# Optimization experiments

Measured on AMD Instinct MI355X. Metric: run time of the kernel, lower is better.

Reference implementation:

```python
import jax, jax.numpy as jnp
import numpy as np

VERIFY_OP = 0  # protocol['operations','verify']
YES = 0        # protocol['concepts','yes']
NO = 1         # protocol['concepts','no']
EMBED_DIM = 16


def _act(x):
    # torch.clamp(x, -1, 5) + 0.1 * x
    return jnp.clip(x, -1.0, 5.0) + 0.1 * x


def setup_inputs() -> dict:
    key = jax.random.key(0)
    ks = jax.random.split(key, 6)
    B, O, Fd, C, L, E = 32, 64, 512, 512, 16, EMBED_DIM
    D2 = 2 * E * E  # 512
    scene = jax.random.normal(ks[0], (B, O, Fd), jnp.float32)
    program_ops = jax.random.randint(ks[1], (B, L), 0, 4)
    program_concepts = jax.random.randint(ks[2], (B, L), 0, C)
    concept_table = jax.random.normal(ks[3], (C, D2), jnp.float32) * 0.02
    feat_W = jax.random.normal(ks[4], (D2, Fd), jnp.float32) * 0.02
    feat_b = jax.random.normal(ks[5], (D2,), jnp.float32) * 0.02
    return {"scene": scene, "program_ops": program_ops,
            "program_concepts": program_concepts, "concept_table": concept_table,
            "feat_W": feat_W, "feat_b": feat_b}


def reference(scene, program_ops, program_concepts, concept_table, feat_W, feat_b):
    B, O, Fd = scene.shape
    C, D2 = concept_table.shape
    E = EMBED_DIM
    sq = E * E
    N = C + O  # num_nodes = max_concepts + num_objects

    # feature_linear on all scenes (all scenes full -> embed_init rows overwritten)
    objects = jnp.einsum('bof,df->bod', scene, feat_W) + feat_b  # [B,O,2sq]
    concepts = jnp.broadcast_to(concept_table[None], (B, C, D2))
    all_nodes = jnp.concatenate([concepts, objects], axis=1)  # [B,N,2sq]
    n1 = all_nodes[..., :sq].reshape(B, N, E, E)
    n2 = all_nodes[..., sq:].reshape(B, N, E, E)
    nodes = jnp.einsum('bnij,bnjk->bnik', n1, n2)  # [B,N,E,E]
    exp_nodes = nodes.reshape(B, N, sq)

    args_emb = concept_table[program_concepts]  # [B,L,2sq]
    L = args_emb.shape[1]
    g1 = args_emb[..., :sq].reshape(B, L, E, E).transpose(1, 0, 2, 3)  # [L,B,E,E]
    g2 = args_emb[..., sq:].reshape(B, L, E, E).transpose(1, 0, 2, 3)
    ops = program_ops.T  # [L,B]

    def step(att, xs):
        a1, a2, op = xs
        # matmul(a1^T, nodes, a2) per node
        wm = jnp.einsum('bji,bnjk,bkl->bnil', a1, nodes, a2).reshape(B, N, sq)
        em = wm * att[:, :, None]
        sim = jnp.einsum('bnd,bmd->bnm', em, exp_nodes)  # [B,N,N]
        if_verify = _act(sim[:, :, YES] - sim[:, :, NO])  # [B,N]
        if_transfer = _act(sim.sum(axis=1))               # [B,N]
        is_verify = (op == VERIFY_OP).astype(att.dtype)[:, None]
        new_att = is_verify * if_verify + (1.0 - is_verify) * if_transfer
        return new_att, new_att

    att0 = jnp.ones((B, N), scene.dtype)
    att, history = jax.lax.scan(step, att0, (g1, g2, ops))
    return jax.nn.log_softmax(att, axis=1), history
```

## Files before the change

kernel.cpp:

```cpp
#include <hip/hip_runtime.h>

#define Bb 32
#define Oo 64
#define FD 512
#define Cc 512
#define Ll 16
#define SQ 256
#define D2 512
#define NN 576
#define QQ 6
#define NPB 96
#define NPW 12
#define STAG 17u

typedef __attribute__((ext_vector_type(8))) short short8v;
typedef __attribute__((ext_vector_type(4))) float f32x4;
typedef unsigned long long u64;

__device__ inline unsigned short bf16_rne(float f) {
  unsigned u = __builtin_bit_cast(unsigned, f);
  unsigned r = (u + 0x7fffu + ((u >> 16) & 1u)) >> 16;
  return (unsigned short)r;
}
__device__ inline float bf16_to_f(unsigned short h) {
  unsigned u = ((unsigned)h) << 16;
  return __builtin_bit_cast(float, u);
}
__device__ inline u64 pack_tag(float v, unsigned tag) {
  return ((u64)__float_as_uint(v) << 32) | (u64)tag;
}

__global__ __launch_bounds__(256) void prep(const float* __restrict__ W,
                                            unsigned short* __restrict__ WH,
                                            unsigned short* __restrict__ WL,
                                            u64* __restrict__ slotG,
                                            u64* __restrict__ slotS) {
  const int gid = blockIdx.x * 256 + threadIdx.x;
#pragma unroll
  for (int k = 0; k < 2; ++k) {
    const int i = gid * 2 + k;
    if (i < Bb * QQ * 2 * SQ)
      __hip_atomic_store(&slotG[i], 0ULL, __ATOMIC_RELAXED, __HIP_MEMORY_SCOPE_AGENT);
  }
  if (gid < Bb * QQ * 2)
    __hip_atomic_store(&slotS[gid], 0ULL, __ATOMIC_RELAXED, __HIP_MEMORY_SCOPE_AGENT);
  const float4 v = ((const float4*)W)[gid];
  float vv[4] = {v.x, v.y, v.z, v.w};
  unsigned short hh[4], ll[4];
#pragma unroll
  for (int j = 0; j < 4; ++j) {
    unsigned short hb = bf16_rne(vv[j]);
    float rem = vv[j] - bf16_to_f(hb);
    hh[j] = hb;
    ll[j] = bf16_rne(rem);
  }
  ushort4 h, lo;
  h.x = hh[0]; h.y = hh[1]; h.z = hh[2]; h.w = hh[3];
  lo.x = ll[0]; lo.y = ll[1]; lo.z = ll[2]; lo.w = ll[3];
  ((ushort4*)WH)[gid] = h;
  ((ushort4*)WL)[gid] = lo;
}

__global__ __launch_bounds__(256) void gemm_nodes(const float* __restrict__ scene,
                                                  const unsigned short* __restrict__ WH,
                                                  const unsigned short* __restrict__ WL,
                                                  const float* __restrict__ bias,
                                                  const float* __restrict__ ct,
                                                  float* __restrict__ cn,
                                                  float* __restrict__ on) {
  __shared__ __align__(16) float sbuf[16 * 529 + 512];
  const int bid = blockIdx.x, tid = threadIdx.x;
  if (bid >= 128) {
    float* ls = sbuf;
    const int c0 = (bid - 128) * 8;
    for (int i = tid; i < 1024; i += 256)
      ((float4*)ls)[i] = ((const float4*)(ct + (size_t)c0 * D2))[i];
    __syncthreads();
    const int n = tid >> 5, sub = tid & 31;
    const float* n1 = &ls[n * 512];
    const float* n2 = &ls[n * 512 + 256];
    float* dst = cn + (size_t)(c0 + n) * SQ + sub * 8;
#pragma unroll
    for (int j = 0; j < 8; ++j) {
      const int e = sub * 8 + j, i = e >> 4, k = e & 15;
      float s = 0.f;
#pragma unroll
      for (int t = 0; t < 16; ++t) s += n1[i * 16 + t] * n2[t * 16 + k];
      dst[j] = s;
    }
    return;
  }
  float (*objLds)[529] = (float(*)[529])sbuf;
  float* biasL = sbuf + 16 * 529;
  const int wave = tid >> 6, lane = tid & 63;
  const int rowbase = bid * 16;
  for (int i = tid; i < 512; i += 256) biasL[i] = bias[i];

  const int ar = lane & 15;
  const int koff = (lane >> 4) * 8;
  const float* Arow = scene + (size_t)(rowbase + ar) * FD;
  const int ncol0 = wave * 128;
  f32x4 acc[8];
#pragma unroll
  for (int i = 0; i < 8; ++i) acc[i] = (f32x4){0.f, 0.f, 0.f, 0.f};

  for (int k0 = 0; k0 < FD; k0 += 32) {
    float a[8];
    *(float4*)&a[0] = *(const float4*)&Arow[k0 + koff];
    *(float4*)&a[4] = *(const float4*)&Arow[k0 + koff + 4];
    short8v ah, al;
#pragma unroll
    for (int j = 0; j < 8; ++j) {
      unsigned short hb = bf16_rne(a[j]);
      float rem = a[j] - bf16_to_f(hb);
      ah[j] = (short)hb;
      al[j] = (short)bf16_rne(rem);
    }
#pragma unroll
    for (int ni = 0; ni < 8; ++ni) {
      const int d = ncol0 + ni * 16 + ar;
      const short8v wh = *(const short8v*)&WH[(size_t)d * FD + k0 + koff];
      const short8v wl = *(const short8v*)&WL[(size_t)d * FD + k0 + koff];
      acc[ni] = __builtin_amdgcn_mfma_f32_16x16x32_bf16(ah, wh, acc[ni], 0, 0, 0);
      acc[ni] = __builtin_amdgcn_mfma_f32_16x16x32_bf16(ah, wl, acc[ni], 0, 0, 0);
      acc[ni] = __builtin_amdgcn_mfma_f32_16x16x32_bf16(al, wh, acc[ni], 0, 0, 0);
    }
  }
  __syncthreads();
  const int crow = (lane >> 4) * 4;
  const int ccol = lane & 15;
#pragma unroll
  for (int ni = 0; ni < 8; ++ni) {
    const int d = ncol0 + ni * 16 + ccol;
    const float bv = biasL[d];
#pragma unroll
    for (int r = 0; r < 4; ++r) objLds[crow + r][d] = acc[ni][r] + bv;
  }
  __syncthreads();
  const int o = tid >> 4, ii = tid & 15;
  float n1r[16];
#pragma unroll
  for (int j = 0; j < 16; ++j) n1r[j] = objLds[o][ii * 16 + j];
  float* dst = on + (size_t)(rowbase + o) * SQ + ii * 16;
#pragma unroll
  for (int k = 0; k < 16; ++k) {
    float s = 0.f;
#pragma unroll
    for (int j = 0; j < 16; ++j) s += n1r[j] * objLds[o][256 + j * 16 + k];
    dst[k] = s;
  }
}

__global__ __launch_bounds__(512) void scan8(const int* __restrict__ ops_p,
                                             const int* __restrict__ pcs,
                                             const float* __restrict__ ct,
                                             const float* __restrict__ cn,
                                             const float* __restrict__ on,
                                             float* __restrict__ out,
                                             u64* __restrict__ slotG,
                                             u64* __restrict__ slotS) {
  const int b = blockIdx.x & 31;
  const int q = blockIdx.x >> 5;
  const int tid = threadIdx.x, wave = tid >> 6, lane = tid & 63;
  __shared__ __align__(16) float ndl[NPB][SQ];
  __shared__ __align__(16) float Gab[Ll][2 * SQ];
  __shared__ __align__(16) float red[8][SQ];
  __shared__ __align__(16) float gbuf[QQ][SQ];
  __shared__ float hist[Ll][NPB];
  __shared__ __align__(16) float Dls[SQ], Mq[SQ], Tt[SQ];
  __shared__ float attL[NPB];
  __shared__ int opsL[Ll], pcsL[Ll];
  __shared__ float sS[1];

  if (tid < Ll) { opsL[tid] = ops_p[b * Ll + tid]; pcsL[tid] = pcs[b * Ll + tid]; }
  const int n0 = q * NPB;
  for (int idx = tid; idx < NPB * 64; idx += 512) {
    const int r = idx >> 6, c4 = idx & 63;
    const int n = n0 + r;
    const float* src = (n < Cc) ? (cn + (size_t)n * SQ)
                                : (on + ((size_t)b * Oo + (n - Cc)) * SQ);
    *(float4*)&ndl[r][c4 * 4] = *(const float4*)(src + c4 * 4);
  }
  if (tid < SQ) Dls[tid] = cn[tid] - cn[SQ + tid];
  if (tid < NPB) attL[tid] = 1.f;
  __syncthreads();
  for (int idx = tid; idx < Ll * 128; idx += 512) {
    const int l = idx >> 7, j = idx & 127;
    *(float4*)&Gab[l][j * 4] = *(const float4*)&ct[(size_t)pcsL[l] * D2 + j * 4];
  }
  __syncthreads();
#pragma unroll
  for (int li = 0; li < 2; ++li) {
    const int l = wave + li * 8;
    if (opsL[l] == 0) {
      float t4[4];
#pragma unroll
      for (int j = 0; j < 4; ++j) {
        const int e = lane * 4 + j, r = e >> 4, c = e & 15;
        float s = 0.f;
#pragma unroll
        for (int t = 0; t < 16; ++t) s += Dls[r * 16 + t] * Gab[l][SQ + c * 16 + t];
        t4[j] = s;
      }
      *(f32x4*)&red[wave][lane * 4] = *(f32x4*)t4;
      asm volatile("s_waitcnt lgkmcnt(0)" ::: "memory");
      __builtin_amdgcn_sched_barrier(0);
      float g4[4];
#pragma unroll
      for (int j = 0; j < 4; ++j) {
        const int e = lane * 4 + j, r = e >> 4, c = e & 15;
        float s = 0.f;
#pragma unroll
        for (int t = 0; t < 16; ++t) s += Gab[l][r * 16 + t] * red[wave][t * 16 + c];
        g4[j] = s;
      }
      *(f32x4*)&Gab[l][lane * 4] = *(f32x4*)g4;
    }
  }
  f32x4 m = (f32x4){0.f, 0.f, 0.f, 0.f};
#pragma unroll
  for (int ni = 0; ni < NPW; ++ni)
    m += *(const f32x4*)&ndl[wave * NPW + ni][lane * 4];
  __syncthreads();

  int tc = 0;
  for (int l = 0; l < Ll; ++l) {
    const bool verify = (opsL[l] == 0);
    const float* gsrc;
    if (!verify) {
      const int par = tc & 1;
      ++tc;
      const unsigned tg = (unsigned)(l + 1);
      *(f32x4*)&red[wave][lane * 4] = m;
      __syncthreads();
      if (wave == 0) {
        f32x4 s = (f32x4){0.f, 0.f, 0.f, 0.f};
#pragma unroll
        for (int w = 0; w < 8; ++w) s += *(const f32x4*)&red[w][lane * 4];
        *(f32x4*)&Mq[lane * 4] = s;
        asm volatile("s_waitcnt lgkmcnt(0)" ::: "memory");
        __builtin_amdgcn_sched_barrier(0);
        float t4[4];
#pragma unroll
        for (int j = 0; j < 4; ++j) {
          const int e = lane * 4 + j, r = e >> 4, c = e & 15;
          float s2 = 0.f;
#pragma unroll
          for (int t = 0; t < 16; ++t) s2 += Gab[l][t * 16 + r] * Mq[t * 16 + c];
          t4[j] = s2;
        }
        *(f32x4*)&Tt[lane * 4] = *(f32x4*)t4;
        asm volatile("s_waitcnt lgkmcnt(0)" ::: "memory");
        __builtin_amdgcn_sched_barrier(0);
        u64* myslot = slotG + ((size_t)(b * QQ + q) * 2 + par) * SQ;
        float g4[4];
#pragma unroll
        for (int j = 0; j < 4; ++j) {
          const int e = j * 64 + lane, r = e >> 4, c = e & 15;
          float s2 = 0.f;
#pragma unroll
          for (int t = 0; t < 16; ++t) s2 += Tt[r * 16 + t] * Gab[l][SQ + t * 16 + c];
          g4[j] = s2;
          __hip_atomic_store(&myslot[e], pack_tag(s2, tg),
                             __ATOMIC_RELAXED, __HIP_MEMORY_SCOPE_AGENT);
        }
#pragma unroll
        for (int j = 0; j < 4; ++j) gbuf[q][j * 64 + lane] = g4[j];
      } else if (wave <= QQ - 1) {
        const int qq = (q + wave) % QQ;
        const u64* base = slotG + ((size_t)(b * QQ + qq) * 2 + par) * SQ;
        if (lane == 0) {
          while ((unsigned)__hip_atomic_load(base + (SQ - 1), __ATOMIC_RELAXED,
                                             __HIP_MEMORY_SCOPE_AGENT) != tg) {}
        }
        u64 pk[4];
        for (;;) {
#pragma unroll
          for (int j = 0; j < 4; ++j)
            pk[j] = __hip_atomic_load(base + j * 64 + lane, __ATOMIC_RELAXED,
                                      __HIP_MEMORY_SCOPE_AGENT);
          bool ok = true;
#pragma unroll
          for (int j = 0; j < 4; ++j) ok &= ((unsigned)pk[j] == tg);
          if (__all(ok)) break;
        }
#pragma unroll
        for (int j = 0; j < 4; ++j)
          gbuf[qq][j * 64 + lane] = __uint_as_float((unsigned)(pk[j] >> 32));
      }
      __syncthreads();
      f32x4 gg = (f32x4){0.f, 0.f, 0.f, 0.f};
#pragma unroll
      for (int qq = 0; qq < QQ; ++qq) gg += *(const f32x4*)&gbuf[qq][lane * 4];
      f32x4 mn = (f32x4){0.f, 0.f, 0.f, 0.f};
#pragma unroll
      for (int ni = 0; ni < NPW; ++ni) {
        const int nl = wave * NPW + ni;
        const f32x4 v = *(const f32x4*)&ndl[nl][lane * 4];
        float p = v[0] * gg[0] + v[1] * gg[1] + v[2] * gg[2] + v[3] * gg[3];
        p += __shfl_xor(p, 1);  p += __shfl_xor(p, 2);  p += __shfl_xor(p, 4);
        p += __shfl_xor(p, 8);  p += __shfl_xor(p, 16); p += __shfl_xor(p, 32);
        const float na = fminf(fmaxf(p, -1.f), 5.f) + 0.1f * p;
        if (lane == 0) { attL[nl] = na; hist[l][nl] = na; }
        mn[0] += na * v[0]; mn[1] += na * v[1]; mn[2] += na * v[2]; mn[3] += na * v[3];
      }
      m = mn;
    } else {
      const f32x4 g = *(const f32x4*)&Gab[l][lane * 4];
      f32x4 mn = (f32x4){0.f, 0.f, 0.f, 0.f};
#pragma unroll
      for (int ni = 0; ni < NPW; ++ni) {
        const int nl = wave * NPW + ni;
        const f32x4 v = *(const f32x4*)&ndl[nl][lane * 4];
        float p = v[0] * g[0] + v[1] * g[1] + v[2] * g[2] + v[3] * g[3];
        p += __shfl_xor(p, 1);  p += __shfl_xor(p, 2);  p += __shfl_xor(p, 4);
        p += __shfl_xor(p, 8);  p += __shfl_xor(p, 16); p += __shfl_xor(p, 32);
        const float x = attL[nl] * p;
        const float na = fminf(fmaxf(x, -1.f), 5.f) + 0.1f * x;
        if (lane == 0) { attL[nl] = na; hist[l][nl] = na; }
        mn[0] += na * v[0]; mn[1] += na * v[1]; mn[2] += na * v[2]; mn[3] += na * v[3];
      }
      m = mn;
    }
  }
  __syncthreads();

  if (wave == 0) {
    float mv = -1e30f;
    for (int i = lane; i < NPB; i += 64) mv = fmaxf(mv, attL[i]);
    mv = fmaxf(mv, __shfl_xor(mv, 1));  mv = fmaxf(mv, __shfl_xor(mv, 2));
    mv = fmaxf(mv, __shfl_xor(mv, 4));  mv = fmaxf(mv, __shfl_xor(mv, 8));
    mv = fmaxf(mv, __shfl_xor(mv, 16)); mv = fmaxf(mv, __shfl_xor(mv, 32));
    float sv = 0.f;
    for (int i = lane; i < NPB; i += 64) sv += expf(attL[i] - mv);
    sv += __shfl_xor(sv, 1);  sv += __shfl_xor(sv, 2);  sv += __shfl_xor(sv, 4);
    sv += __shfl_xor(sv, 8);  sv += __shfl_xor(sv, 16); sv += __shfl_xor(sv, 32);
    if (lane == 0) {
      __hip_atomic_store(&slotS[(b * QQ + q) * 2 + 0], pack_tag(mv, STAG),
                         __ATOMIC_RELAXED, __HIP_MEMORY_SCOPE_AGENT);
      __hip_atomic_store(&slotS[(b * QQ + q) * 2 + 1], pack_tag(sv, STAG),
                         __ATOMIC_RELAXED, __HIP_MEMORY_SCOPE_AGENT);
    }
    const int role = (lane < QQ) ? 0 : ((lane >= 8 && lane < 8 + QQ) ? 1 : -1);
    const int sidx = (role == 0) ? ((b * QQ + lane) * 2)
                                 : ((role == 1) ? ((b * QQ + (lane - 8)) * 2 + 1) : 0);
    u64 pk;
    for (;;) {
      pk = (role >= 0) ? __hip_atomic_load(&slotS[sidx], __ATOMIC_RELAXED,
                                           __HIP_MEMORY_SCOPE_AGENT)
                       : (u64)STAG;
      if (__all((unsigned)pk == STAG)) break;
    }
    const float v = __uint_as_float((unsigned)(pk >> 32));
    float gM = -1e30f, gT = 0.f;
#pragma unroll
    for (int qq = 0; qq < QQ; ++qq) gM = fmaxf(gM, __shfl(v, qq));
#pragma unroll
    for (int qq = 0; qq < QQ; ++qq)
      gT += __shfl(v, 8 + qq) * expf(__shfl(v, qq) - gM);
    if (lane == 0) sS[0] = gM + logf(gT);
  }
  __syncthreads();
  const float lse = sS[0];
  if (tid < NPB) out[(size_t)b * NN + n0 + tid] = attL[tid] - lse;
  for (int idx = tid; idx < Ll * NPB; idx += 512) {
    const int l = idx / NPB, i = idx - l * NPB;
    out[(size_t)Bb * NN + ((size_t)l * Bb + b) * NN + n0 + i] = hist[l][i];
  }
}

extern "C" void kernel_launch(void* const* d_in, const int* in_sizes, int n_in,
                              void* d_out, int out_size, void* d_ws, size_t ws_size,
                              hipStream_t stream) {
  const float* scene = (const float*)d_in[0];
  const int* ops = (const int*)d_in[1];
  const int* pcs = (const int*)d_in[2];
  const float* ct = (const float*)d_in[3];
  const float* fW = (const float*)d_in[4];
  const float* fb = (const float*)d_in[5];
  float* out = (float*)d_out;
  float* ws = (float*)d_ws;

  float* cn = ws;
  float* on = cn + (size_t)Cc * SQ;
  unsigned short* WH = (unsigned short*)(on + (size_t)Bb * Oo * SQ);
  unsigned short* WL = WH + (size_t)D2 * FD;
  u64* slotG = (u64*)(WL + (size_t)D2 * FD);
  u64* slotS = slotG + (size_t)Bb * QQ * 2 * SQ;

  prep<<<256, 256, 0, stream>>>(fW, WH, WL, slotG, slotS);
  gemm_nodes<<<192, 256, 0, stream>>>(scene, WH, WL, fb, ct, cn, on);
  scan8<<<Bb * QQ, 512, 0, stream>>>(ops, pcs, ct, cn, on, out, slotG, slotS);
}
```

Measured before the change: 142.4 us.

## Exchange partial node sums across blocks before the transfer matmuls instead of after

In the transfer branch, each block now publishes its raw partial weighted node sum M through the cross-block slots rather than the finished a1^T M a2 product. Every wave then sums all partial M vectors and computes the two 16x16 matmuls redundantly, using a vectorised layout with four outputs per lane. This shortens the serial work wave 0 does before publishing and removes one matmul chain from the critical path between blocks. Attention values are also kept in registers instead of shared memory. The trade is that all eight waves now repeat the small matmuls on every transfer step.

Measured after the change: 157.6 us. +10.7%, slower.

```diff
diff --git a/kernel.cpp b/kernel.cpp
--- a/kernel.cpp
+++ b/kernel.cpp
@@ -182,7 +182,6 @@
     *(float4*)&ndl[r][c4 * 4] = *(const float4*)(src + c4 * 4);
   }
   if (tid < SQ) Dls[tid] = cn[tid] - cn[SQ + tid];
-  if (tid < NPB) attL[tid] = 1.f;
   __syncthreads();
   for (int idx = tid; idx < Ll * 128; idx += 512) {
     const int l = idx >> 7, j = idx & 127;
@@ -196,10 +195,10 @@
       float t4[4];
 #pragma unroll
       for (int j = 0; j < 4; ++j) {
-        const int e = lane * 4 + j, r = e >> 4, c = e & 15;
+        const int e = lane * 4 + j, rr = e >> 4, c = e & 15;
         float s = 0.f;
 #pragma unroll
-        for (int t = 0; t < 16; ++t) s += Dls[r * 16 + t] * Gab[l][SQ + c * 16 + t];
+        for (int t = 0; t < 16; ++t) s += Dls[rr * 16 + t] * Gab[l][SQ + c * 16 + t];
         t4[j] = s;
       }
       *(f32x4*)&red[wave][lane * 4] = *(f32x4*)t4;
@@ -208,10 +207,10 @@
       float g4[4];
 #pragma unroll
       for (int j = 0; j < 4; ++j) {
-        const int e = lane * 4 + j, r = e >> 4, c = e & 15;
+        const int e = lane * 4 + j, rr = e >> 4, c = e & 15;
         float s = 0.f;
 #pragma unroll
-        for (int t = 0; t < 16; ++t) s += Gab[l][r * 16 + t] * red[wave][t * 16 + c];
+        for (int t = 0; t < 16; ++t) s += Gab[l][rr * 16 + t] * red[wave][t * 16 + c];
         g4[j] = s;
       }
       *(f32x4*)&Gab[l][lane * 4] = *(f32x4*)g4;
@@ -223,49 +222,29 @@
     m += *(const f32x4*)&ndl[wave * NPW + ni][lane * 4];
   __syncthreads();
 
+  float att[NPW];
+#pragma unroll
+  for (int ni = 0; ni < NPW; ++ni) att[ni] = 1.f;
+
+  const int r16 = lane >> 2, c0 = (lane & 3) * 4;
   int tc = 0;
   for (int l = 0; l < Ll; ++l) {
     const bool verify = (opsL[l] == 0);
-    const float* gsrc;
     if (!verify) {
       const int par = tc & 1;
       ++tc;
       const unsigned tg = (unsigned)(l + 1);
       *(f32x4*)&red[wave][lane * 4] = m;
       __syncthreads();
+      f32x4 s = (f32x4){0.f, 0.f, 0.f, 0.f};
+#pragma unroll
+      for (int w = 0; w < 8; ++w) s += *(const f32x4*)&red[w][lane * 4];
       if (wave == 0) {
-        f32x4 s = (f32x4){0.f, 0.f, 0.f, 0.f};
-#pragma unroll
-        for (int w = 0; w < 8; ++w) s += *(const f32x4*)&red[w][lane * 4];
-        *(f32x4*)&Mq[lane * 4] = s;
-        asm volatile("s_waitcnt lgkmcnt(0)" ::: "memory");
-        __builtin_amdgcn_sched_barrier(0);
-        float t4[4];
-#pragma unroll
-        for (int j = 0; j < 4; ++j) {
-          const int e = lane * 4 + j, r = e >> 4, c = e & 15;
-          float s2 = 0.f;
-#pragma unroll
-          for (int t = 0; t < 16; ++t) s2 += Gab[l][t * 16 + r] * Mq[t * 16 + c];
-          t4[j] = s2;
-        }
-        *(f32x4*)&Tt[lane * 4] = *(f32x4*)t4;
-        asm volatile("s_waitcnt lgkmcnt(0)" ::: "memory");
-        __builtin_amdgcn_sched_barrier(0);
         u64* myslot = slotG + ((size_t)(b * QQ + q) * 2 + par) * SQ;
-        float g4[4];
-#pragma unroll
-        for (int j = 0; j < 4; ++j) {
-          const int e = j * 64 + lane, r = e >> 4, c = e & 15;
-          float s2 = 0.f;
-#pragma unroll
-          for (int t = 0; t < 16; ++t) s2 += Tt[r * 16 + t] * Gab[l][SQ + t * 16 + c];
-          g4[j] = s2;
-          __hip_atomic_store(&myslot[e], pack_tag(s2, tg),
+#pragma unroll
+        for (int j = 0; j < 4; ++j)
+          __hip_atomic_store(&myslot[lane * 4 + j], pack_tag(s[j], tg),
                              __ATOMIC_RELAXED, __HIP_MEMORY_SCOPE_AGENT);
-        }
-#pragma unroll
-        for (int j = 0; j < 4; ++j) gbuf[q][j * 64 + lane] = g4[j];
       } else if (wave <= QQ - 1) {
         const int qq = (q + wave) % QQ;
         const u64* base = slotG + ((size_t)(b * QQ + qq) * 2 + par) * SQ;
@@ -277,7 +256,7 @@
         for (;;) {
 #pragma unroll
           for (int j = 0; j < 4; ++j)
-            pk[j] = __hip_atomic_load(base + j * 64 + lane, __ATOMIC_RELAXED,
+            pk[j] = __hip_atomic_load(base + lane * 4 + j, __ATOMIC_RELAXED,
                                       __HIP_MEMORY_SCOPE_AGENT);
           bool ok = true;
 #pragma unroll
@@ -286,12 +265,37 @@
         }
 #pragma unroll
         for (int j = 0; j < 4; ++j)
-          gbuf[qq][j * 64 + lane] = __uint_as_float((unsigned)(pk[j] >> 32));
+          gbuf[wave][lane * 4 + j] = __uint_as_float((unsigned)(pk[j] >> 32));
       }
       __syncthreads();
+      f32x4 M4 = s;
+#pragma unroll
+      for (int w = 1; w < QQ; ++w) M4 += *(const f32x4*)&gbuf[w][lane * 4];
+      *(f32x4*)&Mq[lane * 4] = M4;
+      asm volatile("s_waitcnt lgkmcnt(0)" ::: "memory");
+      __builtin_amdgcn_sched_barrier(0);
+      f32x4 T4 = (f32x4){0.f, 0.f, 0.f, 0.f};
+#pragma unroll
+      for (int t = 0; t < 16; ++t) {
+        const float a1v = Gab[l][t * 16 + r16];
+        const f32x4 mv = *(const f32x4*)&Mq[t * 16 + c0];
+        T4[0] += a1v * mv[0]; T4[1] += a1v * mv[1];
+        T4[2] += a1v * mv[2]; T4[3] += a1v * mv[3];
+      }
+      *(f32x4*)&Tt[lane * 4] = T4;
+      asm volatile("s_waitcnt lgkmcnt(0)" ::: "memory");
+      __builtin_amdgcn_sched_barrier(0);
+      f32x4 tr[4];
+#pragma unroll
+      for (int k = 0; k < 4; ++k) tr[k] = *(const f32x4*)&Tt[r16 * 16 + k * 4];
       f32x4 gg = (f32x4){0.f, 0.f, 0.f, 0.f};
 #pragma unroll
-      for (int qq = 0; qq < QQ; ++qq) gg += *(const f32x4*)&gbuf[qq][lane * 4];
+      for (int t = 0; t < 16; ++t) {
+        const float trv = tr[t >> 2][t & 3];
+        const f32x4 a2v = *(const f32x4*)&Gab[l][SQ + t * 16 + c0];
+        gg[0] += trv * a2v[0]; gg[1] += trv * a2v[1];
+        gg[2] += trv * a2v[2]; gg[3] += trv * a2v[3];
+      }
       f32x4 mn = (f32x4){0.f, 0.f, 0.f, 0.f};
 #pragma unroll
       for (int ni = 0; ni < NPW; ++ni) {
@@ -301,7 +305,8 @@
         p += __shfl_xor(p, 1);  p += __shfl_xor(p, 2);  p += __shfl_xor(p, 4);
         p += __shfl_xor(p, 8);  p += __shfl_xor(p, 16); p += __shfl_xor(p, 32);
         const float na = fminf(fmaxf(p, -1.f), 5.f) + 0.1f * p;
-        if (lane == 0) { attL[nl] = na; hist[l][nl] = na; }
+        att[ni] = na;
+        if (lane == 0) hist[l][nl] = na;
         mn[0] += na * v[0]; mn[1] += na * v[1]; mn[2] += na * v[2]; mn[3] += na * v[3];
       }
       m = mn;
@@ -315,13 +320,18 @@
         float p = v[0] * g[0] + v[1] * g[1] + v[2] * g[2] + v[3] * g[3];
         p += __shfl_xor(p, 1);  p += __shfl_xor(p, 2);  p += __shfl_xor(p, 4);
         p += __shfl_xor(p, 8);  p += __shfl_xor(p, 16); p += __shfl_xor(p, 32);
-        const float x = attL[nl] * p;
+        const float x = att[ni] * p;
         const float na = fminf(fmaxf(x, -1.f), 5.f) + 0.1f * x;
-        if (lane == 0) { attL[nl] = na; hist[l][nl] = na; }
+        att[ni] = na;
+        if (lane == 0) hist[l][nl] = na;
         mn[0] += na * v[0]; mn[1] += na * v[1]; mn[2] += na * v[2]; mn[3] += na * v[3];
       }
       m = mn;
     }
+  }
+  if (lane == 0) {
+#pragma unroll
+    for (int ni = 0; ni < NPW; ++ni) attL[wave * NPW + ni] = att[ni];
   }
   __syncthreads();
 
```
